# Kernel optimization log

Measured on AMD Instinct MI355X. Metric: run time of the kernel, lower is better.

## Reference

```python
import math
import jax, jax.numpy as jnp
from jax import lax
import numpy as np

D = 128            # head_dim
B = 16             # independent KV streams (e.g., heads)
S = 4096           # update sequence length
P = 4096           # reconstruction positions
MAX_SEQ_LEN = 8192
# (n_waves, ema_rate, freq_low, freq_high) per level, coarse -> fine
LEVELS = [(16, 0.001, 0.01, 1.0), (32, 0.005, 0.5, 3.0), (64, 0.02, 1.0, 6.0), (128, 0.05, 2.0, 10.0), (256, 0.1, 4.0, 20.0)]
TWO_PI = 2.0 * math.pi


def setup_inputs() -> dict:
    key = jax.random.key(0)
    ks = jax.random.split(key, 2 + len(LEVELS))
    inp = {}
    inp['kv_vectors'] = jax.random.normal(ks[0], (B, S, D), dtype=jnp.float32)
    inp['positions'] = jnp.arange(S, dtype=jnp.int32)
    inp['recon_positions'] = jnp.sort(jax.random.randint(ks[1], (P,), 0, MAX_SEQ_LEN, dtype=jnp.int32))
    for i, (n, a, lo, hi) in enumerate(LEVELS):
        k1, k2 = jax.random.split(ks[2 + i], 2)
        inp[f'W_enc_{i}'] = jax.random.normal(k1, (3 * n, D), dtype=jnp.float32) / math.sqrt(D)
        inp[f'W_dec_{i}'] = jax.random.normal(k2, (D, n), dtype=jnp.float32) / math.sqrt(n)
        inp[f'base_freqs_{i}'] = jnp.linspace(lo, hi, n, dtype=jnp.float32)
    return inp


def _ema_final(x, alpha):
    # x: [S, ...]; returns EMA state after S sequential steps from zero init.
    def step(c, xt):
        return (1.0 - alpha) * c + alpha * xt, None
    final, _ = lax.scan(step, jnp.zeros(x.shape[1:], x.dtype), x)
    return final


def _forward(kv_vectors, positions, recon_positions, params):
    pos_norm = positions.astype(jnp.float32)[:, None] / MAX_SEQ_LEN    # [S,1]
    rpos_norm = recon_positions.astype(jnp.float32)[:, None] / MAX_SEQ_LEN  # [P,1]
    out = jnp.zeros((kv_vectors.shape[0], recon_positions.shape[0], D), jnp.float32)
    for (n, alpha, _lo, _hi), (W_enc, W_dec, base_freqs) in zip(LEVELS, params):
        deltas = jnp.einsum('bsd,wd->bsw', kv_vectors, W_enc)          # [B,S,3n]
        d_freq, d_amp, d_phase = jnp.split(deltas, 3, axis=-1)         # each [B,S,n]
        pos_signal = jnp.sin(base_freqs[None, :] * pos_norm * TWO_PI)  # [S,n]
        xs = jnp.stack([d_freq * pos_signal[None], jnp.abs(d_amp), d_phase], axis=0)  # [3,B,S,n]
        xs = jnp.transpose(xs, (2, 0, 1, 3))                           # [S,3,B,n]
        freqs, amps, phases = _ema_final(xs, alpha)                    # each [B,n]
        wave_phases = TWO_PI * (freqs[:, None, :] + base_freqs[None, None, :]) * rpos_norm[None] + phases[:, None, :]
        wave_values = amps[:, None, :] * jnp.sin(wave_phases)          # [B,P,n]
        out = out + jnp.einsum('bpn,dn->bpd', wave_values, W_dec)
    return out


def reference(kv_vectors, positions, recon_positions,
              W_enc_0, W_dec_0, base_freqs_0,
              W_enc_1, W_dec_1, base_freqs_1,
              W_enc_2, W_dec_2, base_freqs_2,
              W_enc_3, W_dec_3, base_freqs_3,
              W_enc_4, W_dec_4, base_freqs_4):
    params = [(W_enc_0, W_dec_0, base_freqs_0), (W_enc_1, W_dec_1, base_freqs_1),
              (W_enc_2, W_dec_2, base_freqs_2), (W_enc_3, W_dec_3, base_freqs_3),
              (W_enc_4, W_dec_4, base_freqs_4)]
    return _forward(kv_vectors, positions, recon_positions, params)
```

## Files before the change

### kernel.cpp

```cpp
#include <hip/hip_runtime.h>

typedef __attribute__((ext_vector_type(8))) short short8;
typedef __attribute__((ext_vector_type(4))) float floatx4;
typedef __attribute__((ext_vector_type(4))) int intx4;

#define NLEV 5
#define B_   16
#define S_   4096
#define D_   128
#define P_   4096
#define CTOT 496
#define BP   (B_ * CTOT)
#define NBX  64
#define WPADG 512
#define INV2PI 0.15915494309189535f
#define NJBLK 336

__device__ __forceinline__ unsigned cvtpk(float a, float b) {
    unsigned r;
    asm("v_cvt_pk_bf16_f32 %0, %1, %2" : "=v"(r) : "v"(a), "v"(b));
    return r;
}

__global__ __launch_bounds__(256) void encoder(
    const float* __restrict__ kv, const int* __restrict__ positions,
    const float* __restrict__ we0, const float* __restrict__ we1,
    const float* __restrict__ we2, const float* __restrict__ we3,
    const float* __restrict__ we4,
    const float* __restrict__ wd0, const float* __restrict__ wd1,
    const float* __restrict__ wd2, const float* __restrict__ wd3,
    const float* __restrict__ wd4,
    const float* __restrict__ bfr0, const float* __restrict__ bfr1,
    const float* __restrict__ bfr2, const float* __restrict__ bfr3,
    const float* __restrict__ bfr4,
    unsigned short* __restrict__ wdbT,
    float* __restrict__ accb)
{
    __shared__ unsigned short kvb[64 * 136];
    __shared__ float pf[64];
    const int b   = blockIdx.y;
    const int bid = blockIdx.x;
    const int tid = threadIdx.x;

    if (b == 0 && bid < 64) {
        int e0 = (bid * 256 + tid) * 4;
        int d = e0 >> 9, w = e0 & 511;
        float4 v4 = {0.f, 0.f, 0.f, 0.f};
        if (w < CTOT) {
            const float* src; int off, nl;
            if (w < 16)       { src = wd0; off = 0;   nl = 16;  }
            else if (w < 48)  { src = wd1; off = 16;  nl = 32;  }
            else if (w < 112) { src = wd2; off = 48;  nl = 64;  }
            else if (w < 240) { src = wd3; off = 112; nl = 128; }
            else              { src = wd4; off = 240; nl = 256; }
            v4 = *(const float4*)(src + (size_t)d * nl + (w - off));
        }
        *(unsigned long long*)&wdbT[e0] =
            (unsigned long long)cvtpk(v4.x, v4.y)
            | ((unsigned long long)cvtpk(v4.z, v4.w) << 32);
    }

    int bx, lb;
    if (bid < 96)       { bx = bid / 24;            lb = bid % 24; }
    else if (bid < 144) { int r = bid - 96;  bx = 4 + r / 12; lb = r % 12; }
    else if (bid < 192) { int r = bid - 144; bx = 8 + r / 6;  lb = r % 6;  }
    else                { int r = bid - 192; bx = 16 + r / 3; lb = r % 3;  }
    const int t0 = S_ - 64 * (bx + 1);

    const float* src = kv + ((size_t)(b * S_ + t0)) * D_;
    #pragma unroll
    for (int f = 0; f < 8; ++f) {
        int idx = f * 256 + tid;
        int t = idx >> 5, d4 = idx & 31;
        float4 val = *(const float4*)(src + t * D_ + d4 * 4);
        *(unsigned long long*)&kvb[t * 136 + d4 * 4] =
            (unsigned long long)cvtpk(val.x, val.y)
            | ((unsigned long long)cvtpk(val.z, val.w) << 32);
    }
    if (tid < 64) pf[tid] = (float)positions[t0 + tid] * (1.0f / 8192.0f);
    __syncthreads();

    const int wid = tid >> 6, lane = tid & 63, ln = lane & 15, quad = lane >> 4;

    const int cnt = 9 + (bx < 16 ? 12 : 0) + (bx < 8 ? 24 : 0) + (bx < 4 ? 48 : 0);
    int jid = lb * 4 + wid;
    if (jid >= cnt) return;

    const int   n_l[5]  = {16, 32, 64, 128, 256};
    const int   coff[5] = {0, 16, 48, 112, 240};
    const float al[5]   = {0.001f, 0.005f, 0.02f, 0.05f, 0.1f};
    const float l2m[5]  = {-0.0014434169f, -0.0072315692f, -0.0291463449f,
                           -0.0740005794f, -0.1520030934f};
    const float* bfp[5] = {bfr0, bfr1, bfr2, bfr3, bfr4};
    const float* wep[5] = {we0, we1, we2, we3, we4};

    int l = 0, ci = jid;
    {
        const int sz[5] = {3, 6, (bx < 16 ? 12 : 0), (bx < 8 ? 24 : 0), (bx < 4 ? 48 : 0)};
        #pragma unroll
        for (int q = 0; q < 4; ++q) {
            if (ci >= sz[l]) { ci -= sz[l]; ++l; }
        }
    }
    const int n = n_l[l];

    const float* wrow = wep[l] + (size_t)(ci * 16 + ln) * D_;
    floatx4 acc[4];
    #pragma unroll
    for (int m = 0; m < 4; ++m) acc[m] = (floatx4){0.f, 0.f, 0.f, 0.f};
    #pragma unroll
    for (int k = 0; k < 4; ++k) {
        float4 wa = *(const float4*)(wrow + k * 32 + quad * 8);
        float4 wb = *(const float4*)(wrow + k * 32 + quad * 8 + 4);
        intx4 bi = { (int)cvtpk(wa.x, wa.y), (int)cvtpk(wa.z, wa.w),
                     (int)cvtpk(wb.x, wb.y), (int)cvtpk(wb.z, wb.w) };
        short8 bfg = *(short8*)&bi;
        #pragma unroll
        for (int m = 0; m < 4; ++m) {
            short8 af = *(const short8*)&kvb[(m * 16 + ln) * 136 + k * 32 + quad * 8];
            acc[m] = __builtin_amdgcn_mfma_f32_16x16x32_bf16(af, bfg, acc[m], 0, 0, 0);
        }
    }

    const int kind  = (ci * 16) / n;
    const int local = ci * 16 + ln - kind * n;
    const float bsv = (kind == 0) ? bfp[l][local] : 0.0f;

    const float l2 = l2m[l];
    const float fs = exp2f(-l2);
    const float fq = exp2f(-(float)(quad * 4) * l2);
    const float em = exp2f(-16.0f * l2);
    float fr[4];
    fr[0] = fq; fr[1] = fq * fs; fr[2] = fr[1] * fs; fr[3] = fr[2] * fs;
    float Cm = al[l] * exp2f((float)(S_ - 1 - t0) * l2);

    float s = 0.0f;
    #pragma unroll
    for (int m = 0; m < 4; ++m) {
        #pragma unroll
        for (int r = 0; r < 4; ++r) {
            int   trel = m * 16 + quad * 4 + r;
            float wt   = Cm * fr[r];
            float v    = acc[m][r];
            if (kind == 0) {
                float rev = bsv * pf[trel];
                rev = __builtin_amdgcn_fractf(rev);
                v *= __builtin_amdgcn_sinf(rev);
            } else if (kind == 1) {
                v = fabsf(v);
            }
            s += wt * v;
        }
        Cm *= em;
    }
    s += __shfl_xor(s, 16);
    s += __shfl_xor(s, 32);
    if (lane < 16)
        accb[((size_t)bx * 3 + kind) * BP + b * CTOT + coff[l] + local] = s;
}

__global__ __launch_bounds__(256) void decoder(
    const float* __restrict__ accb,
    const unsigned short* __restrict__ wdbT, const int* __restrict__ rpos,
    const float* __restrict__ b0, const float* __restrict__ b1,
    const float* __restrict__ b2, const float* __restrict__ b3,
    const float* __restrict__ b4,
    float* __restrict__ out)
{
    __shared__ unsigned short v[64 * 264];
    __shared__ float rpn[64];
    const int b = blockIdx.y, p0 = blockIdx.x * 64, tid = threadIdx.x;
    if (tid < 64) rpn[tid] = (float)rpos[p0 + tid] * (1.0f / 8192.0f);

    const int wid = tid >> 6, lane = tid & 63, ln = lane & 15, quad = lane >> 4;
    const int nt0 = wid * 2;

    floatx4 acc[4][2];
    #pragma unroll
    for (int m = 0; m < 4; ++m)
        #pragma unroll
        for (int j = 0; j < 2; ++j) acc[m][j] = (floatx4){0.f, 0.f, 0.f, 0.f};

    #pragma unroll
    for (int half = 0; half < 2; ++half) {
        const int w0 = half * 256;
        const int w = w0 + tid;
        float A = 0.f, Q = 0.f, Ph = 0.f;
        if (w < CTOT) {
            const float* bf; int off;
            if (w < 16)       { bf = b0; off = 0;   }
            else if (w < 48)  { bf = b1; off = 16;  }
            else if (w < 112) { bf = b2; off = 48;  }
            else if (w < 240) { bf = b3; off = 112; }
            else              { bf = b4; off = 240; }
            const int parts = (w < 48) ? 64 : (w < 112) ? 16 : (w < 240) ? 8 : 4;
            float f = 0.f, Aa = 0.f, ph = 0.f;
            const float* pp = accb + b * CTOT + w;
            for (int x = 0; x < parts; ++x) {
                f  += pp[0];
                Aa += pp[BP];
                ph += pp[2 * BP];
                pp += 3 * (size_t)BP;
            }
            A  = Aa;
            Q  = f + bf[w - off];
            Ph = ph * INV2PI;
        }
        __syncthreads();
        for (int p = 0; p < 64; p += 2) {
            float r0 = __builtin_amdgcn_fractf(fmaf(Q, rpn[p],     Ph));
            float r1 = __builtin_amdgcn_fractf(fmaf(Q, rpn[p + 1], Ph));
            float s0 = A * __builtin_amdgcn_sinf(r0);
            float s1 = A * __builtin_amdgcn_sinf(r1);
            unsigned pk = cvtpk(s0, s1);
            v[p * 264 + tid]       = (unsigned short)pk;
            v[(p + 1) * 264 + tid] = (unsigned short)(pk >> 16);
        }
        __syncthreads();

        #pragma unroll
        for (int kk = 0; kk < 8; ++kk) {
            short8 bn[2];
            #pragma unroll
            for (int j = 0; j < 2; ++j)
                bn[j] = *(const short8*)(wdbT + (size_t)((nt0 + j) * 16 + ln) * WPADG
                                         + w0 + kk * 32 + quad * 8);
            short8 am[4];
            #pragma unroll
            for (int m = 0; m < 4; ++m)
                am[m] = *(const short8*)&v[(m * 16 + ln) * 264 + kk * 32 + quad * 8];
            #pragma unroll
            for (int m = 0; m < 4; ++m)
                #pragma unroll
                for (int j = 0; j < 2; ++j)
                    acc[m][j] = __builtin_amdgcn_mfma_f32_16x16x32_bf16(
                                    am[m], bn[j], acc[m][j], 0, 0, 0);
        }
    }

    #pragma unroll
    for (int m = 0; m < 4; ++m)
        #pragma unroll
        for (int j = 0; j < 2; ++j)
            #pragma unroll
            for (int r = 0; r < 4; ++r) {
                int p = p0 + m * 16 + quad * 4 + r;
                int d = (nt0 + j) * 16 + ln;
                out[((size_t)(b * P_ + p)) * D_ + d] = acc[m][j][r];
            }
}

extern "C" void kernel_launch(void* const* d_in, const int* in_sizes, int n_in,
                              void* d_out, int out_size, void* d_ws, size_t ws_size,
                              hipStream_t stream)
{
    const float* kv        = (const float*)d_in[0];
    const int*   positions = (const int*)d_in[1];
    const int*   rpos      = (const int*)d_in[2];

    char* ws = (char*)d_ws;
    float*          accb  = (float*)(ws + 0);
    unsigned short* wdbT  = (unsigned short*)(ws + 6094848);

    encoder<<<dim3(NJBLK, B_), 256, 0, stream>>>(
        kv, positions,
        (const float*)d_in[3], (const float*)d_in[6], (const float*)d_in[9],
        (const float*)d_in[12], (const float*)d_in[15],
        (const float*)d_in[4], (const float*)d_in[7], (const float*)d_in[10],
        (const float*)d_in[13], (const float*)d_in[16],
        (const float*)d_in[5], (const float*)d_in[8], (const float*)d_in[11],
        (const float*)d_in[14], (const float*)d_in[17],
        wdbT, accb);

    decoder<<<dim3(P_ / 64, B_), 256, 0, stream>>>(
        accb, wdbT, rpos,
        (const float*)d_in[5], (const float*)d_in[8], (const float*)d_in[11],
        (const float*)d_in[14], (const float*)d_in[17],
        (float*)d_out);
}
```

Before: 174.7 us.

## Reduce encoder partials via atomics and swizzle decoder LDS wave-value tile

The encoder now atomically accumulates its per-block partial EMA sums into a single zeroed buffer, replacing a per-block partials array that the decoder had to sum serially over up to 64 parts. The decoder then does one vectorized float4 load per four waves. Its wave-value staging is also restructured so each lane computes four consecutive waves for 16 positions, with a 64-bit XOR-swizzled LDS write instead of a padded layout. This costs a memset launch and atomic contention, and makes the summation order nondeterministic.

```diff
diff --git a/kernel.cpp b/kernel.cpp
--- a/kernel.cpp
+++ b/kernel.cpp
@@ -11,7 +11,6 @@
 #define P_   4096
 #define CTOT 496
 #define BP   (B_ * CTOT)
-#define NBX  64
 #define WPADG 512
 #define INV2PI 0.15915494309189535f
 #define NJBLK 336
@@ -156,7 +155,7 @@
     s += __shfl_xor(s, 16);
     s += __shfl_xor(s, 32);
     if (lane < 16)
-        accb[((size_t)bx * 3 + kind) * BP + b * CTOT + coff[l] + local] = s;
+        atomicAdd(accb + (size_t)kind * BP + b * CTOT + coff[l] + local, s);
 }
 
 __global__ __launch_bounds__(256) void decoder(
@@ -167,13 +166,14 @@
     const float* __restrict__ b4,
     float* __restrict__ out)
 {
-    __shared__ unsigned short v[64 * 264];
+    __shared__ unsigned short v[64 * 256];
     __shared__ float rpn[64];
     const int b = blockIdx.y, p0 = blockIdx.x * 64, tid = threadIdx.x;
     if (tid < 64) rpn[tid] = (float)rpos[p0 + tid] * (1.0f / 8192.0f);
 
     const int wid = tid >> 6, lane = tid & 63, ln = lane & 15, quad = lane >> 4;
     const int nt0 = wid * 2;
+    char* vb = (char*)v;
 
     floatx4 acc[4][2];
     #pragma unroll
@@ -184,37 +184,43 @@
     #pragma unroll
     for (int half = 0; half < 2; ++half) {
         const int w0 = half * 256;
-        const int w = w0 + tid;
-        float A = 0.f, Q = 0.f, Ph = 0.f;
-        if (w < CTOT) {
+        const int wbase = w0 + lane * 4;
+        float Qv[4], Av[4], Pv[4];
+        if (wbase < CTOT) {
             const float* bf; int off;
-            if (w < 16)       { bf = b0; off = 0;   }
-            else if (w < 48)  { bf = b1; off = 16;  }
-            else if (w < 112) { bf = b2; off = 48;  }
-            else if (w < 240) { bf = b3; off = 112; }
-            else              { bf = b4; off = 240; }
-            const int parts = (w < 48) ? 64 : (w < 112) ? 16 : (w < 240) ? 8 : 4;
-            float f = 0.f, Aa = 0.f, ph = 0.f;
-            const float* pp = accb + b * CTOT + w;
-            for (int x = 0; x < parts; ++x) {
-                f  += pp[0];
-                Aa += pp[BP];
-                ph += pp[2 * BP];
-                pp += 3 * (size_t)BP;
-            }
-            A  = Aa;
-            Q  = f + bf[w - off];
-            Ph = ph * INV2PI;
+            if (wbase < 16)       { bf = b0; off = 0;   }
+            else if (wbase < 48)  { bf = b1; off = 16;  }
+            else if (wbase < 112) { bf = b2; off = 48;  }
+            else if (wbase < 240) { bf = b3; off = 112; }
+            else                  { bf = b4; off = 240; }
+            float4 ff = *(const float4*)(accb + 0 * BP + b * CTOT + wbase);
+            float4 aa = *(const float4*)(accb + 1 * BP + b * CTOT + wbase);
+            float4 pp = *(const float4*)(accb + 2 * BP + b * CTOT + wbase);
+            float4 bb = *(const float4*)(bf + (wbase - off));
+            Qv[0] = ff.x + bb.x; Qv[1] = ff.y + bb.y;
+            Qv[2] = ff.z + bb.z; Qv[3] = ff.w + bb.w;
+            Av[0] = aa.x; Av[1] = aa.y; Av[2] = aa.z; Av[3] = aa.w;
+            Pv[0] = pp.x * INV2PI; Pv[1] = pp.y * INV2PI;
+            Pv[2] = pp.z * INV2PI; Pv[3] = pp.w * INV2PI;
+        } else {
+            #pragma unroll
+            for (int j = 0; j < 4; ++j) { Qv[j] = 0.f; Av[j] = 0.f; Pv[j] = 0.f; }
         }
         __syncthreads();
-        for (int p = 0; p < 64; p += 2) {
-            float r0 = __builtin_amdgcn_fractf(fmaf(Q, rpn[p],     Ph));
-            float r1 = __builtin_amdgcn_fractf(fmaf(Q, rpn[p + 1], Ph));
-            float s0 = A * __builtin_amdgcn_sinf(r0);
-            float s1 = A * __builtin_amdgcn_sinf(r1);
-            unsigned pk = cvtpk(s0, s1);
-            v[p * 264 + tid]       = (unsigned short)pk;
-            v[(p + 1) * 264 + tid] = (unsigned short)(pk >> 16);
+
+        #pragma unroll 4
+        for (int pr = 0; pr < 16; ++pr) {
+            const int p = wid * 16 + pr;
+            const float rp = rpn[p];
+            float s0 = Av[0] * __builtin_amdgcn_sinf(__builtin_amdgcn_fractf(fmaf(Qv[0], rp, Pv[0])));
+            float s1 = Av[1] * __builtin_amdgcn_sinf(__builtin_amdgcn_fractf(fmaf(Qv[1], rp, Pv[1])));
+            float s2 = Av[2] * __builtin_amdgcn_sinf(__builtin_amdgcn_fractf(fmaf(Qv[2], rp, Pv[2])));
+            float s3 = Av[3] * __builtin_amdgcn_sinf(__builtin_amdgcn_fractf(fmaf(Qv[3], rp, Pv[3])));
+            unsigned long long u = (unsigned long long)cvtpk(s0, s1)
+                                 | ((unsigned long long)cvtpk(s2, s3) << 32);
+            int byte = p * 512 + lane * 8;
+            byte ^= (p & 7) << 4;
+            *(unsigned long long*)(vb + byte) = u;
         }
         __syncthreads();
 
@@ -227,8 +233,11 @@
                                          + w0 + kk * 32 + quad * 8);
             short8 am[4];
             #pragma unroll
-            for (int m = 0; m < 4; ++m)
-                am[m] = *(const short8*)&v[(m * 16 + ln) * 264 + kk * 32 + quad * 8];
+            for (int m = 0; m < 4; ++m) {
+                int byte = (m * 16 + ln) * 512 + kk * 64 + quad * 16;
+                byte ^= (ln & 7) << 4;
+                am[m] = *(const short8*)(vb + byte);
+            }
             #pragma unroll
             for (int m = 0; m < 4; ++m)
                 #pragma unroll
@@ -260,7 +269,9 @@
 
     char* ws = (char*)d_ws;
     float*          accb  = (float*)(ws + 0);
-    unsigned short* wdbT  = (unsigned short*)(ws + 6094848);
+    unsigned short* wdbT  = (unsigned short*)(ws + 95232);
+
+    hipMemsetAsync(accb, 0, (size_t)(3 * BP) * sizeof(float), stream);
 
     encoder<<<dim3(NJBLK, B_), 256, 0, stream>>>(
         kv, positions,
```

Result: faster. 161.3 us (-7.7%).
